# Optimization experiments

Measured on AMD Instinct MI355X. Metric: run time of the kernel, lower is better.

The kernel has to match this reference:

```python
import jax, jax.numpy as jnp
import numpy as np

HEADS = 8
EPS = 1e-6

def conv1x1(x, W, b):
    # x: [B,C,H,W], W: [O,C], b: [O]
    return jnp.einsum('oc,bchw->bohw', W, x) + b[None, :, None, None]

def cross_attn(qf, kf, vf, Wq, bq, Wk, bk, Wv, bv, Wo, bo):
    B, C, H, W = qf.shape
    hd = C // HEADS
    Q = conv1x1(qf, Wq, bq).reshape(B, HEADS, hd, H * W)
    K = conv1x1(kf, Wk, bk).reshape(B, HEADS, hd, H * W)
    V = conv1x1(vf, Wv, bv).reshape(B, HEADS, hd, H * W)
    # contraction over spatial dim -> [B, heads, hd, hd] scores (faithful to source einsum)
    scores = jnp.einsum('bnhd,bnkd->bnhk', Q, K) * (hd ** -0.5)
    attn = jax.nn.softmax(scores, axis=-1)
    out = jnp.einsum('bnhk,bnkd->bnhd', attn, V).reshape(B, C, H, W)
    return conv1x1(out, Wo, bo)

def se_block(x, W1, b1, W2, b2):
    pooled = jnp.mean(x, axis=(2, 3), keepdims=True)  # [B,C,1,1]
    y = jax.nn.relu(conv1x1(pooled, W1, b1))
    return jax.nn.sigmoid(conv1x1(y, W2, b2))

def l2norm_c(x):
    n = jnp.sqrt(jnp.sum(x * x, axis=1, keepdims=True))
    return x / (n + EPS)

def setup_inputs() -> dict:
    key = jax.random.key(0)
    ks = jax.random.split(key, 24)
    B, C, H, W = 8, 512, 64, 64
    r = 16
    s = 0.02
    inp = {
        'rgb_features': jax.random.normal(ks[0], (B, C, H, W), jnp.float32),
        'depth_features': jax.random.normal(ks[1], (B, C, H, W), jnp.float32),
        'lidar_features': jax.random.normal(ks[2], (B, C, H, W), jnp.float32),
        # 6 cross-modal attention modules, stacked (all same channel sizes)
        # order: rgb->depth, rgb->lidar, depth->rgb, depth->lidar, lidar->rgb, lidar->depth
        'attn_Wq': jax.random.normal(ks[3], (6, C, C), jnp.float32) * s,
        'attn_bq': jnp.zeros((6, C), jnp.float32),
        'attn_Wk': jax.random.normal(ks[4], (6, C, C), jnp.float32) * s,
        'attn_bk': jnp.zeros((6, C), jnp.float32),
        'attn_Wv': jax.random.normal(ks[5], (6, C, C), jnp.float32) * s,
        'attn_bv': jnp.zeros((6, C), jnp.float32),
        'attn_Wo': jax.random.normal(ks[6], (6, C, C), jnp.float32) * s,
        'attn_bo': jnp.zeros((6, C), jnp.float32),
        # SE blocks for rgb/depth/lidar, stacked
        'se_W1': jax.random.normal(ks[7], (3, C // r, C), jnp.float32) * s,
        'se_b1': jnp.zeros((3, C // r), jnp.float32),
        'se_W2': jax.random.normal(ks[8], (3, C, C // r), jnp.float32) * s,
        'se_b2': jnp.zeros((3, C), jnp.float32),
        'gate_W': jax.random.normal(ks[9], (3, 3 * C + 3), jnp.float32) * s,
        'gate_b': jnp.zeros((3,), jnp.float32),
        'fusion_W': jax.random.normal(ks[10], (3 * C, 3 * C), jnp.float32) * s,
        'fusion_b': jnp.zeros((3 * C,), jnp.float32),
    }
    return inp

def reference(rgb_features, depth_features, lidar_features,
              attn_Wq, attn_bq, attn_Wk, attn_bk, attn_Wv, attn_bv, attn_Wo, attn_bo,
              se_W1, se_b1, se_W2, se_b2, gate_W, gate_b, fusion_W, fusion_b):
    def ca(i, qf, kf, vf):
        return cross_attn(qf, kf, vf,
                          attn_Wq[i], attn_bq[i], attn_Wk[i], attn_bk[i],
                          attn_Wv[i], attn_bv[i], attn_Wo[i], attn_bo[i])
    rgb_cross = rgb_features + ca(0, rgb_features, depth_features, depth_features) \
                             + ca(1, rgb_features, lidar_features, lidar_features)
    depth_cross = depth_features + ca(2, depth_features, rgb_features, rgb_features) \
                                 + ca(3, depth_features, lidar_features, lidar_features)
    lidar_cross = lidar_features + ca(4, lidar_features, rgb_features, rgb_features) \
                                 + ca(5, lidar_features, depth_features, depth_features)

    rgb_refined = l2norm_c(rgb_cross * se_block(rgb_cross, se_W1[0], se_b1[0], se_W2[0], se_b2[0]))
    depth_refined = l2norm_c(depth_cross * se_block(depth_cross, se_W1[1], se_b1[1], se_W2[1], se_b2[1]))
    lidar_refined = l2norm_c(lidar_cross * se_block(lidar_cross, se_W1[2], se_b1[2], se_W2[2], se_b2[2]))

    B, C, H, W = rgb_features.shape
    depth_sparsity = jnp.mean((depth_features == 0).astype(jnp.float32), axis=(1, 2, 3), keepdims=True)
    rgb_variance = jnp.var(rgb_features, axis=(1, 2, 3), keepdims=True, ddof=1)
    lidar_sparsity = jnp.mean((lidar_features == 0).astype(jnp.float32), axis=(1, 2, 3), keepdims=True)
    quality = jnp.concatenate([depth_sparsity, rgb_variance, lidar_sparsity], axis=1)  # [B,3,1,1]
    quality = jnp.broadcast_to(quality, (B, 3, H, W))

    combined = jnp.concatenate([rgb_refined, depth_refined, lidar_refined], axis=1)
    combined_with_metrics = jnp.concatenate([combined, quality], axis=1)
    alpha = jax.nn.sigmoid(conv1x1(combined_with_metrics, gate_W, gate_b))  # [B,3,H,W]

    weighted = jnp.concatenate([
        rgb_refined * alpha[:, 0:1],
        depth_refined * alpha[:, 1:2],
        lidar_refined * alpha[:, 2:3],
    ], axis=1)
    return conv1x1(weighted, fusion_W, fusion_b)
```

## Files before the change

### kernel.cpp

```cpp
#include <hip/hip_runtime.h>
#include <hip/hip_bf16.h>
#include <stdint.h>

using bf16 = __hip_bfloat16;
typedef short bfrag8 __attribute__((ext_vector_type(8)));
typedef float f32x4 __attribute__((ext_vector_type(4)));

constexpr long OFF_XT   = 0L;
constexpr long OFF_XC   = 100663296L;
constexpr long OFF_WQ   = 201326592L;
constexpr long OFF_WK   = 204472320L;
constexpr long OFF_WVT  = 207618048L;
constexpr long OFF_WOB  = 210763776L;
constexpr long OFF_FW   = 213909504L;
constexpr long OFF_BO2  = 218628096L;
constexpr long OFF_POOL = 218646528L;
constexpr long OFF_SE   = 218695680L;
constexpr long OFF_QACC = 218744832L;
constexpr long OFF_CS   = 218745856L;
constexpr long OFF_GB   = 218795008L;
constexpr long OFF_ATT  = 231377920L;
constexpr long OFF_VST  = 234523648L;
constexpr long OFF_QST  = 435850240L;
constexpr long OFF_MVEC = 436243456L;

__device__ __forceinline__ void mfma_bf16(f32x4& c, bfrag8 a, bfrag8 b) {
  asm("v_mfma_f32_16x16x32_bf16 %0, %1, %2, %0" : "+v"(c) : "v"(a), "v"(b));
}

__device__ __forceinline__ void gload16(const void* g, void* l) {
  __builtin_amdgcn_global_load_lds(
      (__attribute__((address_space(1))) void*)(g),
      (__attribute__((address_space(3))) void*)(l), 16, 0, 0);
}

__device__ __forceinline__ float bf2f(short s) {
  union { uint32_t u; float f; } cv;
  cv.u = ((uint32_t)(unsigned short)s) << 16;
  return cv.f;
}

__device__ __forceinline__ void swz_mn(int gy, long& m0, long& n0) {
  const int gx = gridDim.x;
  const int orig = blockIdx.y * gx + blockIdx.x;
  const int q = (gx * gy) >> 3;
  const int wgid = (orig & 7) * q + (orig >> 3);
  m0 = (long)(wgid / gy) * 128;
  n0 = (long)(wgid % gy) * 128;
}

#define SWZ_OFF(r, kb) ((kb) ^ (((r) & 7) << 4))

__device__ __forceinline__ void bar256() {
  __builtin_amdgcn_sched_barrier(0);
  __builtin_amdgcn_s_barrier();
  __builtin_amdgcn_sched_barrier(0);
}

__device__ __forceinline__ void stage_half(const bf16* __restrict__ g, long ldg,
                                           char* slot, int t) {
#pragma unroll
  for (int j = 0; j < 2; ++j) {
    const int L = t * 16 + j * 8192;
    const int r = L >> 7;
    const int kb = (L & 127) ^ ((r & 7) << 4);
    gload16(g + (long)r * ldg + (kb >> 1), slot + L);
  }
}

template<int NT>
__device__ __forceinline__ void gemm256_core(
    const bf16* __restrict__ A, long lda,
    const bf16* __restrict__ B, long ldb,
    long m0, long n0, char* sm, f32x4 (&acc)[4][4][2])
{
  const int t = threadIdx.x;
  const int lane = t & 63, wid = t >> 6;
  const int wm = wid >> 2, wn = wid & 3;
  const int l16 = lane & 15, lk = lane >> 4;

  auto STAGE = [&](int mat, int hf, int kt) {
    const bool wrap = (kt >= NT);
    const int ktw = wrap ? kt - NT : kt;
    const int kp = ktw & 1;
    char* slot = wrap ? (sm + 131072)
                      : (mat == 0 ? sm + (kp * 2 + hf) * 16384
                                  : sm + 65536 + (kp * 2 + hf) * 16384);
    if (mat == 0)
      stage_half(A + (m0 + (long)hf * 128) * lda + ktw * 64, lda, slot, t);
    else
      stage_half(B + (n0 + (long)hf * 128) * ldb + ktw * 64, ldb, slot, t);
  };

  STAGE(0, 0, 0); STAGE(0, 1, 0); STAGE(1, 0, 0); STAGE(1, 1, 0);
  STAGE(1, 1, 1); STAGE(0, 1, 1);
  __builtin_amdgcn_sched_barrier(0);
  asm volatile("s_waitcnt vmcnt(4)" ::: "memory");
  bar256();

  constexpr int s_mat[8] = {0, 1, 1, 0, 0, 1, 1, 0};
  constexpr int s_hf[8]  = {0, 0, 1, 1, 0, 0, 1, 1};
  constexpr int s_dkt[8] = {1, 1, 2, 2, 2, 2, 3, 3};

  bfrag8 af[4][2], bfr0[2][2], bfr1[2][2];

  for (int i = 0; i < NT / 2; ++i) {
#pragma unroll
    for (int p = 0; p < 8; ++p) {
      const int q = p & 3, kp = p >> 2;
      const int ah = (q >= 2) ? 1 : 0;
      const int bh = (q == 1 || q == 2) ? 1 : 0;
      const char* Ab = sm + (kp * 2 + ah) * 16384;
      const char* Bb = sm + 65536 + (kp * 2 + bh) * 16384;
      if (q == 0 || q == 2) {
#pragma unroll
        for (int mf = 0; mf < 4; ++mf) {
          const int rowA = wm * 64 + mf * 16 + l16;
#pragma unroll
          for (int ks = 0; ks < 2; ++ks)
            af[mf][ks] = *(const bfrag8*)(Ab + rowA * 128 +
                                          SWZ_OFF(rowA, ks * 64 + lk * 16));
        }
      }
      if (q == 0) {
#pragma unroll
        for (int nf = 0; nf < 2; ++nf) {
          const int rowB = wn * 32 + nf * 16 + l16;
#pragma unroll
          for (int ks = 0; ks < 2; ++ks)
            bfr0[nf][ks] = *(const bfrag8*)(Bb + rowB * 128 +
                                            SWZ_OFF(rowB, ks * 64 + lk * 16));
        }
      }
      if (q == 1) {
#pragma unroll
        for (int nf = 0; nf < 2; ++nf) {
          const int rowB = wn * 32 + nf * 16 + l16;
#pragma unroll
          for (int ks = 0; ks < 2; ++ks)
            bfr1[nf][ks] = *(const bfrag8*)(Bb + rowB * 128 +
                                            SWZ_OFF(rowB, ks * 64 + lk * 16));
        }
      }
      STAGE(s_mat[p], s_hf[p], 2 * i + s_dkt[p]);
      bar256();
      __builtin_amdgcn_s_setprio(1);
      if (q == 0 || q == 3) {
#pragma unroll
        for (int ks = 0; ks < 2; ++ks)
#pragma unroll
          for (int mf = 0; mf < 4; ++mf)
#pragma unroll
            for (int nf = 0; nf < 2; ++nf)
              mfma_bf16(acc[q][mf][nf], af[mf][ks], bfr0[nf][ks]);
      } else {
#pragma unroll
        for (int ks = 0; ks < 2; ++ks)
#pragma unroll
          for (int mf = 0; mf < 4; ++mf)
#pragma unroll
            for (int nf = 0; nf < 2; ++nf)
              mfma_bf16(acc[q][mf][nf], af[mf][ks], bfr1[nf][ks]);
      }
      __builtin_amdgcn_s_setprio(0);
      if (p == 3 || p == 7) {
        __builtin_amdgcn_sched_barrier(0);
        asm volatile("s_waitcnt vmcnt(4)" ::: "memory");
      }
      bar256();
    }
  }
}

__global__ __launch_bounds__(512, 2) void fusion_gemm256(
    const bf16* __restrict__ A, const bf16* __restrict__ Bt,
    float* __restrict__ Cf, const float* __restrict__ bias)
{
  __shared__ __align__(16) char sm[147456];
  const int orig = blockIdx.y * 128 + blockIdx.x;
  const int wgid = (orig & 7) * 96 + (orig >> 3);
  const long m0 = (long)(wgid / 6) * 256;
  const long n0 = (long)(wgid % 6) * 256;
  f32x4 acc[4][4][2];
#pragma unroll
  for (int q = 0; q < 4; ++q)
#pragma unroll
    for (int mf = 0; mf < 4; ++mf)
#pragma unroll
      for (int nf = 0; nf < 2; ++nf)
        acc[q][mf][nf] = f32x4{0.f, 0.f, 0.f, 0.f};
  gemm256_core<24>(A, 1536, Bt, 1536, m0, n0, sm, acc);

  const int t = threadIdx.x;
  const int lane = t & 63, wid = t >> 6;
  const int wm = wid >> 2, wn = wid & 3;
  const int l16 = lane & 15, lk = lane >> 4;
  constexpr int s_ah[4] = {0, 0, 1, 1};
  constexpr int s_bh[4] = {0, 1, 1, 0};
  const long b = m0 >> 12;
#pragma unroll
  for (int q = 0; q < 4; ++q) {
    const int ah = s_ah[q], bh = s_bh[q];
#pragma unroll
    for (int mf = 0; mf < 4; ++mf) {
      const long row = m0 + ah * 128 + wm * 64 + mf * 16 + lk * 4;
      const long p = row & 4095;
#pragma unroll
      for (int nf = 0; nf < 2; ++nf) {
        const long gc = n0 + bh * 128 + wn * 32 + nf * 16 + l16;
        const float bb = bias[gc];
        float4 o4;
        o4.x = acc[q][mf][nf][0] + bb; o4.y = acc[q][mf][nf][1] + bb;
        o4.z = acc[q][mf][nf][2] + bb; o4.w = acc[q][mf][nf][3] + bb;
        *(float4*)(Cf + b * 6291456L + gc * 4096L + p) = o4;
      }
    }
  }
}

__global__ __launch_bounds__(256) void transpose_kernel(
    const float* __restrict__ x0, const float* __restrict__ x1,
    const float* __restrict__ x2, bf16* __restrict__ xT, bf16* __restrict__ xC,
    float* __restrict__ cs, float* __restrict__ qstage)
{
  __shared__ float tile[32][33];
  __shared__ float qpart[4][2];
  const int zz = blockIdx.z;
  const int m = zz >> 3, b = zz & 7;
  const float* x = (m == 0) ? x0 : (m == 1) ? x1 : x2;
  bf16* y = xT + (long)m * 16777216;
  bf16* y2 = xC + (long)m * 16777216;
  const int p0 = blockIdx.x * 32, c0 = blockIdx.y * 32;
  const int tx = threadIdx.x, ty = threadIdx.y;
  float csp[4];
  float qa = 0.f, qb_ = 0.f;
#pragma unroll
  for (int j = 0; j < 4; ++j) {
    const float v = x[((long)b * 512 + c0 + ty + j * 8) * 4096 + p0 + tx];
    tile[ty + j * 8][tx] = v;
    y2[(long)(c0 + ty + j * 8) * 32768 + (long)b * 4096 + p0 + tx] = __float2bfloat16(v);
    csp[j] = v;
    if (m == 0) { qa += v; qb_ += v * v; }
    else qa += (v == 0.0f) ? 1.0f : 0.0f;
  }
  __syncthreads();
#pragma unroll
  for (int j = 0; j < 4; ++j)
    y[((long)b * 4096 + p0 + ty + j * 8) * 512 + c0 + tx] =
        __float2bfloat16(tile[tx][ty + j * 8]);
#pragma unroll
  for (int j = 0; j < 4; ++j) {
    float s = csp[j];
    for (int o = 16; o; o >>= 1) s += __shfl_xor(s, o);
    if (tx == 0) atomicAdd(&cs[(m * 8 + b) * 512 + c0 + ty + j * 8], s);
  }
  const int t = ty * 32 + tx;
  const int lane = t & 63;
  for (int o = 32; o; o >>= 1) { qa += __shfl_xor(qa, o); qb_ += __shfl_xor(qb_, o); }
  if (lane == 0) { qpart[t >> 6][0] = qa; qpart[t >> 6][1] = qb_; }
  __syncthreads();
  if (t == 0) {
    const float pa = qpart[0][0] + qpart[1][0] + qpart[2][0] + qpart[3][0];
    const float pb = qpart[0][1] + qpart[1][1] + qpart[2][1] + qpart[3][1];
    float* qs = qstage + ((long)zz * 2048 + blockIdx.y * 128 + blockIdx.x) * 2;
    qs[0] = pa; qs[1] = pb;
  }
}

__global__ __launch_bounds__(256) void quality_reduce(
    const float* __restrict__ qstage, float* __restrict__ qacc)
{
  __shared__ float pr[4][2];
  const int zz = blockIdx.x;
  const int m = zz >> 3, b = zz & 7;
  const int t = threadIdx.x;
  float sa = 0.f, sb = 0.f;
  for (int i = t; i < 2048; i += 256) {
    sa += qstage[((long)zz * 2048 + i) * 2];
    sb += qstage[((long)zz * 2048 + i) * 2 + 1];
  }
  for (int o = 32; o; o >>= 1) { sa += __shfl_xor(sa, o); sb += __shfl_xor(sb, o); }
  if ((t & 63) == 0) { pr[t >> 6][0] = sa; pr[t >> 6][1] = sb; }
  __syncthreads();
  if (t == 0) {
    sa = pr[0][0] + pr[1][0] + pr[2][0] + pr[3][0];
    sb = pr[0][1] + pr[1][1] + pr[2][1] + pr[3][1];
    if (m == 0) { qacc[b * 4 + 1] = sa; qacc[b * 4 + 2] = sb; }
    else if (m == 1) qacc[b * 4 + 0] = sa;
    else qacc[b * 4 + 3] = sa;
  }
}

__global__ void prep_weights(
    const float* __restrict__ wq, const float* __restrict__ wk,
    const float* __restrict__ wv, const float* __restrict__ wo,
    const float* __restrict__ fw, const float* __restrict__ bo,
    bf16* __restrict__ wqB, bf16* __restrict__ wkB, bf16* __restrict__ wvT,
    bf16* __restrict__ woB, bf16* __restrict__ fwB, float* __restrict__ bo2)
{
  const long stride = (long)gridDim.x * blockDim.x;
  for (long j = (long)blockIdx.x * blockDim.x + threadIdx.x; j < 2359296; j += stride) {
    fwB[j] = __float2bfloat16(fw[j]);
    if (j < 1572864) {
      wqB[j] = __float2bfloat16(wq[j]);
      wkB[j] = __float2bfloat16(wk[j]);
      woB[j] = __float2bfloat16(wo[j]);
      const long i = j >> 18, rem = j & 262143, cin = rem >> 9, ef = rem & 511;
      wvT[j] = __float2bfloat16(wv[(i << 18) + (ef << 9) + cin]);
    }
    if (j < 1536) {
      const long m2 = j >> 9, cc = j & 511;
      bo2[j] = bo[((m2 * 2) << 9) + cc] + bo[((m2 * 2 + 1) << 9) + cc];
    }
  }
}

template<int BM, int BN>
__device__ __forceinline__ void gemm_core(
    const bf16* __restrict__ A, long lda,
    const bf16* __restrict__ Bt, long ldb,
    int K, long m0, long n0,
    bf16* As, bf16* Bs, f32x4 (&acc)[BM / 32][BN / 32])
{
  constexpr int WM = BM / 2, WN = BN / 2, FM = BM / 32, FN = BN / 32;
  const int t = threadIdx.x;
  const int lane = t & 63, wv = t >> 6;
  const int wr = wv >> 1, wc = wv & 1;
  const int l16 = lane & 15, lk = lane >> 4;
  const int srow = t >> 2;
  const int scol = (t & 3) * 8;
  const bf16* Ag = A + (m0 + srow) * lda + scol;
  const bf16* Bg = Bt + (n0 + srow) * ldb + scol;
  char* AsB = (char*)As;
  char* BsB = (char*)Bs;
  const int aoff = wv * 1024;
  for (int kk = 0; kk < K; kk += 32) {
#pragma unroll
    for (int it = 0; it < BM / 64; ++it)
      gload16(Ag + (long)it * 64 * lda + kk, AsB + it * 4096 + aoff);
#pragma unroll
    for (int it = 0; it < BN / 64; ++it)
      gload16(Bg + (long)it * 64 * ldb + kk, BsB + it * 4096 + aoff);
    __syncthreads();
    bfrag8 af[FM], bfr[FN];
#pragma unroll
    for (int m = 0; m < FM; ++m)
      af[m] = *(const bfrag8*)(AsB + ((wr * WM + m * 16 + l16) * 32 + lk * 8) * 2);
#pragma unroll
    for (int n = 0; n < FN; ++n)
      bfr[n] = *(const bfrag8*)(BsB + ((wc * WN + n * 16 + l16) * 32 + lk * 8) * 2);
#pragma unroll
    for (int m = 0; m < FM; ++m)
#pragma unroll
      for (int n = 0; n < FN; ++n)
        mfma_bf16(acc[m][n], af[m], bfr[n]);
    __syncthreads();
  }
}

__global__ __launch_bounds__(256, 2) void cross_gemm(
    const bf16* __restrict__ xT, const bf16* __restrict__ Weff,
    bf16* __restrict__ crossB, const float* __restrict__ bo2,
    const float* __restrict__ mvec, float* __restrict__ pooled)
{
  __shared__ __align__(16) bf16 As[128 * 32];
  __shared__ __align__(16) bf16 Bs[128 * 32];
  const int z = blockIdx.z;
  const int qm = z >> 3, b = z & 7;
  const int KM0[3] = {1, 0, 0}, KM1[3] = {2, 2, 1};
  const bf16* A0 = xT + (long)KM0[qm] * 16777216 + (long)b * 2097152;
  const bf16* A1 = xT + (long)KM1[qm] * 16777216 + (long)b * 2097152;
  const bf16* B0 = Weff + ((long)(2 * qm) * 8 + b) * 262144;
  const bf16* B1 = Weff + ((long)(2 * qm + 1) * 8 + b) * 262144;
  const bf16* residT = xT + (long)qm * 16777216;
  bf16* Cb = crossB + (long)qm * 16777216;
  f32x4 acc[4][4];
#pragma unroll
  for (int m = 0; m < 4; ++m)
#pragma unroll
    for (int n = 0; n < 4; ++n)
      acc[m][n] = f32x4{0.f, 0.f, 0.f, 0.f};
  long m0, n0;
  swz_mn(4, m0, n0);
  gemm_core<128, 128>(A0, 512, B0, 512, 512, m0, n0, As, Bs, acc);
  gemm_core<128, 128>(A1, 512, B1, 512, 512, m0, n0, As, Bs, acc);

  const int t = threadIdx.x;
  const int lane = t & 63, wv = t >> 6;
  const int wr = wv >> 1, wc = wv & 1;
  const int l16 = lane & 15, lk = lane >> 4;
  const float* mv0 = mvec + ((long)(2 * qm) * 8 + b) * 512;
  const float* mv1 = mvec + ((long)(2 * qm + 1) * 8 + b) * 512;
  float csum[4] = {0.f, 0.f, 0.f, 0.f};
#pragma unroll
  for (int m = 0; m < 4; ++m) {
    const long p = m0 + wr * 64 + m * 16 + lk * 4;
    const long gr0 = (long)b * 4096 + p;
#pragma unroll
    for (int n = 0; n < 4; ++n) {
      const long gc = n0 + wc * 64 + n * 16 + l16;
      const float bb = bo2[qm * 512 + gc] + mv0[gc] + mv1[gc];
#pragma unroll
      for (int i2 = 0; i2 < 4; ++i2) {
        const float rv = __bfloat162float(residT[(gr0 + i2) * 512 + gc]);
        const float o = acc[m][n][i2] + bb + rv;
        Cb[(gr0 + i2) * 512 + gc] = __float2bfloat16(o);
        csum[n] += o;
      }
    }
  }
#pragma unroll
  for (int n = 0; n < 4; ++n) {
    float s = csum[n];
    s += __shfl_xor(s, 16);
    s += __shfl_xor(s, 32);
    if (lane < 16) {
      const long gc = n0 + wc * 64 + n * 16 + l16;
      atomicAdd(&pooled[((long)qm * 8 + b) * 512 + gc], s);
    }
  }
}

__global__ __launch_bounds__(256, 2) void gram_kernel(
    const bf16* __restrict__ xC, bf16* __restrict__ Gb)
{
  __shared__ __align__(16) bf16 As[128 * 32];
  __shared__ __align__(16) bf16 Bs[128 * 32];
  const int z = blockIdx.z;
  const int pair = z >> 3, b = z & 7;
  const int A1[3] = {0, 0, 1}, A2[3] = {1, 2, 2};
  const bf16* A = xC + (long)A1[pair] * 16777216 + b * 4096;
  const bf16* Bt = xC + (long)A2[pair] * 16777216 + b * 4096;
  f32x4 acc[4][4];
#pragma unroll
  for (int m = 0; m < 4; ++m)
#pragma unroll
    for (int n = 0; n < 4; ++n)
      acc[m][n] = f32x4{0.f, 0.f, 0.f, 0.f};
  const long m0 = (long)blockIdx.x * 128, n0 = (long)blockIdx.y * 128;
  gemm_core<128, 128>(A, 32768, Bt, 32768, 4096, m0, n0, As, Bs, acc);
  bf16* C = Gb + (long)z * 262144;
  const int t = threadIdx.x;
  const int lane = t & 63, wv = t >> 6;
  const int wr = wv >> 1, wc = wv & 1;
  const int l16 = lane & 15, lk = lane >> 4;
#pragma unroll
  for (int m = 0; m < 4; ++m) {
    const long gr0 = m0 + wr * 64 + m * 16 + lk * 4;
#pragma unroll
    for (int n = 0; n < 4; ++n) {
      const long gc = n0 + wc * 64 + n * 16 + l16;
#pragma unroll
      for (int i = 0; i < 4; ++i)
        C[(gr0 + i) * 512 + gc] = __float2bfloat16(acc[m][n][i]);
    }
  }
}

__global__ __launch_bounds__(256, 2) void scores_kernel(
    const bf16* __restrict__ wqB, const bf16* __restrict__ wkB,
    const bf16* __restrict__ Gb, const float* __restrict__ colsum,
    const float* __restrict__ bq, const float* __restrict__ bk,
    bf16* __restrict__ attnT)
{
  __shared__ __align__(16) bf16 RtS[64 * 520];
  __shared__ float uv[128];
  __shared__ __align__(16) bf16 attT[64][64];
  const int h = blockIdx.x, b = blockIdx.y, i = blockIdx.z;
  const int qm = i >> 1, jj = i & 1;
  const int km = jj ? (qm == 2 ? 1 : 2) : (qm == 0 ? 1 : 0);
  const int lo = qm < km ? qm : km, hi = qm < km ? km : qm;
  const int pair = lo + hi - 1;
  const int trans = qm > km;
  const bf16* G = Gb + ((long)(pair * 8 + b)) * 262144;
  const bf16* Wq_h = wqB + (long)i * 262144 + h * 64 * 512;
  const bf16* Wk_h = wkB + (long)i * 262144 + h * 64 * 512;
  const bf16* WA = trans ? Wk_h : Wq_h;
  const bf16* WB = trans ? Wq_h : Wk_h;
  const int t = threadIdx.x, lane = t & 63, wv = t >> 6;
  const int l16 = lane & 15, lk = lane >> 4;

  if (t < 128) {
    const int d = t & 63;
    const bf16* wrow = ((t < 64) ? Wq_h : Wk_h) + d * 512;
    const float* sv = colsum + (((t < 64) ? qm : km) * 8 + b) * 512;
    float a = 0.f;
    for (int c = 0; c < 512; c += 8) {
      const bfrag8 w8 = *(const bfrag8*)(wrow + c);
#pragma unroll
      for (int e = 0; e < 8; ++e) a += bf2f(w8[e]) * sv[c + e];
    }
    uv[t] = a;
  }

  f32x4 acc[8][4];
#pragma unroll
  for (int m = 0; m < 8; ++m)
#pragma unroll
    for (int n = 0; n < 4; ++n)
      acc[m][n] = f32x4{0.f, 0.f, 0.f, 0.f};
  for (int kk = 0; kk < 512; kk += 32) {
    bfrag8 a[8], bb[4];
#pragma unroll
    for (int m = 0; m < 8; ++m)
      a[m] = *(const bfrag8*)(G + (wv * 128 + m * 16 + l16) * 512 + kk + lk * 8);
#pragma unroll
    for (int n = 0; n < 4; ++n)
      bb[n] = *(const bfrag8*)(WB + (n * 16 + l16) * 512 + kk + lk * 8);
#pragma unroll
    for (int m = 0; m < 8; ++m)
#pragma unroll
      for (int n = 0; n < 4; ++n)
        mfma_bf16(acc[m][n], a[m], bb[n]);
  }
#pragma unroll
  for (int m = 0; m < 8; ++m)
#pragma unroll
    for (int n = 0; n < 4; ++n)
#pragma unroll
      for (int idx = 0; idx < 4; ++idx)
        RtS[(n * 16 + l16) * 520 + wv * 128 + m * 16 + lk * 4 + idx] =
            __float2bfloat16(acc[m][n][idx]);
  __syncthreads();

  f32x4 acc2[4];
#pragma unroll
  for (int m = 0; m < 4; ++m) acc2[m] = f32x4{0.f, 0.f, 0.f, 0.f};
  for (int kk = 0; kk < 512; kk += 32) {
    bfrag8 a2[4];
#pragma unroll
    for (int m = 0; m < 4; ++m)
      a2[m] = *(const bfrag8*)(WA + (m * 16 + l16) * 512 + kk + lk * 8);
    const bfrag8 b2 = *(const bfrag8*)(&RtS[(wv * 16 + l16) * 520 + kk + lk * 8]);
#pragma unroll
    for (int m = 0; m < 4; ++m) mfma_bf16(acc2[m], a2[m], b2);
  }
  __syncthreads();
  float* S = (float*)RtS;
#pragma unroll
  for (int m = 0; m < 4; ++m)
#pragma unroll
    for (int idx = 0; idx < 4; ++idx)
      S[(m * 16 + lk * 4 + idx) * 68 + wv * 16 + l16] = acc2[m][idx];
  __syncthreads();

  const int r = t >> 2, q = t & 3;
  const float* bq_h = bq + i * 512 + h * 64;
  const float* bk_h = bk + i * 512 + h * 64;
  const float u_r = uv[r], bq_r = bq_h[r];
  float vals[16];
  float mx = -1e30f;
#pragma unroll
  for (int kq = 0; kq < 16; ++kq) {
    const int k = q * 16 + kq;
    float s = trans ? S[k * 68 + r] : S[r * 68 + k];
    s += u_r * bk_h[k] + bq_r * uv[64 + k] + 4096.0f * bq_r * bk_h[k];
    s *= 0.125f;
    vals[kq] = s;
    mx = fmaxf(mx, s);
  }
  mx = fmaxf(mx, __shfl_xor(mx, 1));
  mx = fmaxf(mx, __shfl_xor(mx, 2));
  float sum = 0.f;
#pragma unroll
  for (int kq = 0; kq < 16; ++kq) { vals[kq] = expf(vals[kq] - mx); sum += vals[kq]; }
  sum += __shfl_xor(sum, 1);
  sum += __shfl_xor(sum, 2);
  const float inv = 1.0f / sum;
#pragma unroll
  for (int kq = 0; kq < 16; ++kq)
    attT[q * 16 + kq][r] = __float2bfloat16(vals[kq] * inv);
  __syncthreads();
  const int er = t >> 2, c16 = (t & 3) * 16;
  bf16* op = attnT + (((long)(i * 8 + b) * 8 + h) * 64 + er) * 64 + c16;
  *(bfrag8*)(op) = *(const bfrag8*)(&attT[er][c16]);
  *(bfrag8*)(op + 8) = *(const bfrag8*)(&attT[er][c16 + 8]);
}

__global__ __launch_bounds__(256, 2) void mfold_kernel(
    const bf16* __restrict__ woB, const bf16* __restrict__ attnT,
    const float* __restrict__ bv, bf16* __restrict__ Mbuf, float* __restrict__ mvec)
{
  __shared__ __align__(16) bf16 As[128 * 32];
  __shared__ __align__(16) bf16 Bs[64 * 32];
  const int ib = blockIdx.z;
  const int i = ib >> 3;
  const int h = blockIdx.y;
  const bf16* A = woB + (long)i * 262144 + h * 64;
  const bf16* Bt = attnT + ((long)ib * 8 + h) * 4096;
  f32x4 acc[4][2];
#pragma unroll
  for (int m = 0; m < 4; ++m)
#pragma unroll
    for (int n = 0; n < 2; ++n)
      acc[m][n] = f32x4{0.f, 0.f, 0.f, 0.f};
  const long m0 = (long)blockIdx.x * 128;
  gemm_core<128, 64>(A, 512, Bt, 64, 64, m0, 0, As, Bs, acc);

  const int t = threadIdx.x;
  const int lane = t & 63, wv = t >> 6;
  const int wr = wv >> 1, wc = wv & 1;
  const int l16 = lane & 15, lk = lane >> 4;
  bf16* C = Mbuf + (long)ib * 262144;
  const float* bvp = bv + i * 512 + h * 64;
  float mp[4][4];
#pragma unroll
  for (int m = 0; m < 4; ++m)
#pragma unroll
    for (int i2 = 0; i2 < 4; ++i2) mp[m][i2] = 0.f;
#pragma unroll
  for (int m = 0; m < 4; ++m) {
    const long gr0 = m0 + wr * 64 + m * 16 + lk * 4;
#pragma unroll
    for (int n = 0; n < 2; ++n) {
      const int gc = wc * 32 + n * 16 + l16;
      const float bvv = bvp[gc];
#pragma unroll
      for (int i2 = 0; i2 < 4; ++i2) {
        C[(gr0 + i2) * 512 + h * 64 + gc] = __float2bfloat16(acc[m][n][i2]);
        mp[m][i2] += acc[m][n][i2] * bvv;
      }
    }
  }
#pragma unroll
  for (int m = 0; m < 4; ++m)
#pragma unroll
    for (int i2 = 0; i2 < 4; ++i2) {
      float v = mp[m][i2];
      v += __shfl_xor(v, 1); v += __shfl_xor(v, 2);
      v += __shfl_xor(v, 4); v += __shfl_xor(v, 8);
      if (l16 == 0)
        atomicAdd(&mvec[(long)ib * 512 + m0 + wr * 64 + m * 16 + lk * 4 + i2], v);
    }
}

__global__ __launch_bounds__(256, 2) void weff_gemm(
    const bf16* __restrict__ Mbuf, const bf16* __restrict__ wvT,
    bf16* __restrict__ Weff)
{
  __shared__ __align__(16) bf16 As[128 * 32];
  __shared__ __align__(16) bf16 Bs[128 * 32];
  const int ib = blockIdx.z;
  const int i = ib >> 3;
  f32x4 acc[4][4];
#pragma unroll
  for (int m = 0; m < 4; ++m)
#pragma unroll
    for (int n = 0; n < 4; ++n)
      acc[m][n] = f32x4{0.f, 0.f, 0.f, 0.f};
  const long m0 = (long)blockIdx.x * 128, n0 = (long)blockIdx.y * 128;
  gemm_core<128, 128>(Mbuf + (long)ib * 262144, 512, wvT + (long)i * 262144, 512,
                      512, m0, n0, As, Bs, acc);
  bf16* C = Weff + (long)ib * 262144;
  const int t = threadIdx.x;
  const int lane = t & 63, wv = t >> 6;
  const int wr = wv >> 1, wc = wv & 1;
  const int l16 = lane & 15, lk = lane >> 4;
#pragma unroll
  for (int m = 0; m < 4; ++m) {
    const long gr0 = m0 + wr * 64 + m * 16 + lk * 4;
#pragma unroll
    for (int n = 0; n < 4; ++n) {
      const long gc = n0 + wc * 64 + n * 16 + l16;
#pragma unroll
      for (int i2 = 0; i2 < 4; ++i2)
        C[(gr0 + i2) * 512 + gc] = __float2bfloat16(acc[m][n][i2]);
    }
  }
}

__global__ __launch_bounds__(512) void se_mlp(
    const float* __restrict__ pooled,
    const float* __restrict__ W1, const float* __restrict__ b1,
    const float* __restrict__ W2, const float* __restrict__ b2,
    float* __restrict__ se)
{
  const int b = blockIdx.x, m = blockIdx.y;
  __shared__ float y[32];
  const int t = threadIdx.x;
  if (t < 32) {
    float s = b1[m * 32 + t];
    const float* w = W1 + (long)(m * 32 + t) * 512;
    const float* p = pooled + ((long)m * 8 + b) * 512;
    for (int c = 0; c < 512; ++c) s += w[c] * (p[c] * (1.0f / 4096.0f));
    y[t] = fmaxf(s, 0.0f);
  }
  __syncthreads();
  float s = b2[m * 512 + t];
  const float* w2 = W2 + (long)(m * 512 + t) * 32;
#pragma unroll
  for (int j = 0; j < 32; ++j) s += w2[j] * y[j];
  se[((long)m * 8 + b) * 512 + t] = 1.0f / (1.0f + expf(-s));
}

__global__ __launch_bounds__(384) void refine_gate(
    const bf16* __restrict__ cr0, const bf16* __restrict__ cr1,
    const bf16* __restrict__ cr2, const float* __restrict__ se,
    const float* __restrict__ gw, const float* __restrict__ gb,
    const float* __restrict__ qacc, bf16* __restrict__ weighted)
{
  __shared__ float part[2][3][3];
  const int t = threadIdx.x, wv = t >> 6, lane = t & 63;
  const int px_i = (wv >= 3) ? 1 : 0;
  const int m = wv - px_i * 3;
  const int pix = blockIdx.x * 2 + px_i;
  const int b = pix >> 12;
  const bf16* cr = (m == 0) ? cr0 : (m == 1) ? cr1 : cr2;
  const int c0 = lane * 8;
  const bfrag8 v8 = *(const bfrag8*)(cr + (long)pix * 512 + c0);
  const float* sp = se + ((long)m * 8 + b) * 512 + c0;
  const float4 s0 = *(const float4*)(sp);
  const float4 s1 = *(const float4*)(sp + 4);
  float w[8] = {bf2f(v8[0]) * s0.x, bf2f(v8[1]) * s0.y,
                bf2f(v8[2]) * s0.z, bf2f(v8[3]) * s0.w,
                bf2f(v8[4]) * s1.x, bf2f(v8[5]) * s1.y,
                bf2f(v8[6]) * s1.z, bf2f(v8[7]) * s1.w};
  float ss = 0.f;
#pragma unroll
  for (int i = 0; i < 8; ++i) ss += w[i] * w[i];
  for (int o = 32; o; o >>= 1) ss += __shfl_xor(ss, o);
  const float inv = 1.0f / (sqrtf(ss) + 1e-6f);
  float rf[8];
#pragma unroll
  for (int i = 0; i < 8; ++i) rf[i] = w[i] * inv;

  float a0 = 0.f, a1 = 0.f, a2 = 0.f;
#pragma unroll
  for (int i = 0; i < 8; ++i) {
    const int c = m * 512 + c0 + i;
    a0 += gw[c] * rf[i];
    a1 += gw[1539 + c] * rf[i];
    a2 += gw[3078 + c] * rf[i];
  }
  for (int o = 32; o; o >>= 1) {
    a0 += __shfl_xor(a0, o); a1 += __shfl_xor(a1, o); a2 += __shfl_xor(a2, o);
  }
  if (lane == 0) {
    part[px_i][m][0] = a0; part[px_i][m][1] = a1; part[px_i][m][2] = a2;
  }
  __syncthreads();
  const float N = 2097152.0f;
  const float q0 = qacc[b * 4 + 0] / N;
  const float q1 = (qacc[b * 4 + 2] - qacc[b * 4 + 1] * qacc[b * 4 + 1] / N) / (N - 1.0f);
  const float q2 = qacc[b * 4 + 3] / N;
  const float sg = part[px_i][0][m] + part[px_i][1][m] + part[px_i][2][m] + gb[m] +
                   gw[m * 1539 + 1536] * q0 + gw[m * 1539 + 1537] * q1 +
                   gw[m * 1539 + 1538] * q2;
  const float al = 1.0f / (1.0f + expf(-sg));
  __align__(16) bf16 tmp[8];
#pragma unroll
  for (int i = 0; i < 8; ++i) tmp[i] = __float2bfloat16(rf[i] * al);
  *(bfrag8*)(weighted + (long)pix * 1536 + m * 512 + c0) = *(const bfrag8*)tmp;
}

extern "C" void kernel_launch(void* const* d_in, const int* in_sizes, int n_in,
                              void* d_out, int out_size, void* d_ws, size_t ws_size,
                              hipStream_t stream)
{
  (void)in_sizes; (void)n_in; (void)out_size; (void)ws_size;
  const float* rgb   = (const float*)d_in[0];
  const float* depth = (const float*)d_in[1];
  const float* lidar = (const float*)d_in[2];
  const float* wq  = (const float*)d_in[3];
  const float* bq  = (const float*)d_in[4];
  const float* wk  = (const float*)d_in[5];
  const float* bk  = (const float*)d_in[6];
  const float* wvw = (const float*)d_in[7];
  const float* bv  = (const float*)d_in[8];
  const float* wo  = (const float*)d_in[9];
  const float* bo  = (const float*)d_in[10];
  const float* seW1 = (const float*)d_in[11];
  const float* seb1 = (const float*)d_in[12];
  const float* seW2 = (const float*)d_in[13];
  const float* seb2 = (const float*)d_in[14];
  const float* gw  = (const float*)d_in[15];
  const float* gb  = (const float*)d_in[16];
  const float* fw  = (const float*)d_in[17];
  const float* fb  = (const float*)d_in[18];

  char* ws = (char*)d_ws;
  bf16*  xT   = (bf16*)(ws + OFF_XT);
  bf16*  xC   = (bf16*)(ws + OFF_XC);
  bf16*  wqB  = (bf16*)(ws + OFF_WQ);
  bf16*  wkB  = (bf16*)(ws + OFF_WK);
  bf16*  wvT  = (bf16*)(ws + OFF_WVT);
  bf16*  woB  = (bf16*)(ws + OFF_WOB);
  bf16*  fwB  = (bf16*)(ws + OFF_FW);
  float* bo2  = (float*)(ws + OFF_BO2);
  float* pooled = (float*)(ws + OFF_POOL);
  float* seB  = (float*)(ws + OFF_SE);
  float* qacc = (float*)(ws + OFF_QACC);
  float* cs   = (float*)(ws + OFF_CS);
  bf16*  Gb   = (bf16*)(ws + OFF_GB);
  bf16*  attnT = (bf16*)(ws + OFF_ATT);
  float* qstage = (float*)(ws + OFF_QST);
  float* mvec = (float*)(ws + OFF_MVEC);
  bf16*  Mbuf = (bf16*)(ws + OFF_XC);
  bf16*  Weff = (bf16*)(ws + OFF_XC + 25165824L);
  bf16*  crossB = (bf16*)(ws + OFF_VST);

  (void)hipMemsetAsync(ws + OFF_POOL, 0, OFF_CS + 49152 - OFF_POOL, stream);
  (void)hipMemsetAsync(ws + OFF_MVEC, 0, 98304, stream);

  transpose_kernel<<<dim3(128, 16, 24), dim3(32, 8), 0, stream>>>(rgb, depth, lidar,
                                                                  xT, xC, cs, qstage);
  quality_reduce<<<24, 256, 0, stream>>>(qstage, qacc);
  prep_weights<<<2048, 256, 0, stream>>>(wq, wk, wvw, wo, fw, bo,
                                         wqB, wkB, wvT, woB, fwB, bo2);

  gram_kernel<<<dim3(4, 4, 24), 256, 0, stream>>>(xC, Gb);
  scores_kernel<<<dim3(8, 8, 6), 256, 0, stream>>>(wqB, wkB, Gb, cs, bq, bk, attnT);

  mfold_kernel<<<dim3(4, 8, 48), 256, 0, stream>>>(woB, attnT, bv, Mbuf, mvec);
  weff_gemm<<<dim3(4, 4, 48), 256, 0, stream>>>(Mbuf, wvT, Weff);

  cross_gemm<<<dim3(32, 4, 24), 256, 0, stream>>>(xT, Weff, crossB, bo2, mvec, pooled);
  se_mlp<<<dim3(8, 3), 512, 0, stream>>>(pooled, seW1, seb1, seW2, seb2, seB);

  bf16* cross0 = crossB;
  bf16* cross1 = (bf16*)(ws + OFF_VST + 33554432L);
  bf16* cross2 = (bf16*)(ws + OFF_VST + 67108864L);
  bf16* weighted = (bf16*)(ws + OFF_XC);
  refine_gate<<<16384, 384, 0, stream>>>(cross0, cross1, cross2, seB, gw, gb, qacc, weighted);

  fusion_gemm256<<<dim3(128, 6), 512, 0, stream>>>(weighted, fwB, (float*)d_out, fb);
}
```

Baseline: 882.9 us.

## Move cross GEMM onto pipelined 256x256 core with identity-segment residual

Replaces the 128x128 cross_gemm with a 256x256-tile, 512-thread kernel built on the pipelined gemm256_core, which now takes several K segments from different base pointers. The residual add is folded into the GEMM as a third K segment, multiplying the query modality's features by a bf16 identity matrix built in prep_weights. This removes the separate residual read in the epilogue and gains the larger tile and deeper pipeline. The cost is 50% more MFMA work on an identity block, and the grid shrinks to 768 blocks, which may hurt occupancy balance.

```diff
diff --git a/kernel.cpp b/kernel.cpp
--- a/kernel.cpp
+++ b/kernel.cpp
@@ -23,6 +23,7 @@
 constexpr long OFF_VST  = 234523648L;
 constexpr long OFF_QST  = 435850240L;
 constexpr long OFF_MVEC = 436243456L;
+constexpr long OFF_IDB  = 436341760L;
 
 __device__ __forceinline__ void mfma_bf16(f32x4& c, bfrag8 a, bfrag8 b) {
   asm("v_mfma_f32_16x16x32_bf16 %0, %1, %2, %0" : "+v"(c) : "v"(a), "v"(b));
@@ -68,12 +69,13 @@
   }
 }
 
-template<int NT>
+template<int NSEG, int NTSEG>
 __device__ __forceinline__ void gemm256_core(
-    const bf16* __restrict__ A, long lda,
-    const bf16* __restrict__ B, long ldb,
+    const bf16* const* Aseg, long lda,
+    const bf16* const* Bseg, long ldb,
     long m0, long n0, char* sm, f32x4 (&acc)[4][4][2])
 {
+  constexpr int NT = NSEG * NTSEG;
   const int t = threadIdx.x;
   const int lane = t & 63, wid = t >> 6;
   const int wm = wid >> 2, wn = wid & 3;
@@ -82,14 +84,15 @@
   auto STAGE = [&](int mat, int hf, int kt) {
     const bool wrap = (kt >= NT);
     const int ktw = wrap ? kt - NT : kt;
+    const int seg = ktw / NTSEG, ktt = ktw % NTSEG;
     const int kp = ktw & 1;
     char* slot = wrap ? (sm + 131072)
                       : (mat == 0 ? sm + (kp * 2 + hf) * 16384
                                   : sm + 65536 + (kp * 2 + hf) * 16384);
     if (mat == 0)
-      stage_half(A + (m0 + (long)hf * 128) * lda + ktw * 64, lda, slot, t);
+      stage_half(Aseg[seg] + (m0 + (long)hf * 128) * lda + ktt * 64, lda, slot, t);
     else
-      stage_half(B + (n0 + (long)hf * 128) * ldb + ktw * 64, ldb, slot, t);
+      stage_half(Bseg[seg] + (n0 + (long)hf * 128) * ldb + ktt * 64, ldb, slot, t);
   };
 
   STAGE(0, 0, 0); STAGE(0, 1, 0); STAGE(1, 0, 0); STAGE(1, 1, 0);
@@ -189,7 +192,9 @@
 #pragma unroll
       for (int nf = 0; nf < 2; ++nf)
         acc[q][mf][nf] = f32x4{0.f, 0.f, 0.f, 0.f};
-  gemm256_core<24>(A, 1536, Bt, 1536, m0, n0, sm, acc);
+  const bf16* Aseg[1] = {A};
+  const bf16* Bseg[1] = {Bt};
+  gemm256_core<1, 24>(Aseg, 1536, Bseg, 1536, m0, n0, sm, acc);
 
   const int t = threadIdx.x;
   const int lane = t & 63, wid = t >> 6;
@@ -216,6 +221,82 @@
       }
     }
   }
+}
+
+__global__ __launch_bounds__(512, 2) void cross_gemm256(
+    const bf16* __restrict__ xT, const bf16* __restrict__ Weff,
+    const bf16* __restrict__ idB,
+    bf16* __restrict__ crossB, const float* __restrict__ bo2,
+    const float* __restrict__ mvec, float* __restrict__ pooled)
+{
+  __shared__ __align__(16) char sm[147456];
+  const int z = blockIdx.z;
+  const int qm = z >> 3, b = z & 7;
+  const int KM0[3] = {1, 0, 0}, KM1[3] = {2, 2, 1};
+  const bf16* Aseg[3] = {
+      xT + (long)KM0[qm] * 16777216 + (long)b * 2097152,
+      xT + (long)KM1[qm] * 16777216 + (long)b * 2097152,
+      xT + (long)qm * 16777216 + (long)b * 2097152};
+  const bf16* Bseg[3] = {
+      Weff + ((long)(2 * qm) * 8 + b) * 262144,
+      Weff + ((long)(2 * qm + 1) * 8 + b) * 262144,
+      idB};
+  const int orig = blockIdx.y * 16 + blockIdx.x;
+  const int wgid = (orig & 7) * 4 + (orig >> 3);
+  const long m0 = (long)(wgid >> 1) * 256;
+  const long n0 = (long)(wgid & 1) * 256;
+  f32x4 acc[4][4][2];
+#pragma unroll
+  for (int q = 0; q < 4; ++q)
+#pragma unroll
+    for (int mf = 0; mf < 4; ++mf)
+#pragma unroll
+      for (int nf = 0; nf < 2; ++nf)
+        acc[q][mf][nf] = f32x4{0.f, 0.f, 0.f, 0.f};
+  gemm256_core<3, 8>(Aseg, 512, Bseg, 512, m0, n0, sm, acc);
+
+  const int t = threadIdx.x;
+  const int lane = t & 63, wid = t >> 6;
+  const int wm = wid >> 2, wn = wid & 3;
+  const int l16 = lane & 15, lk = lane >> 4;
+  constexpr int s_ah[4] = {0, 0, 1, 1};
+  constexpr int s_bh[4] = {0, 1, 1, 0};
+  bf16* Cb = crossB + (long)qm * 16777216;
+  const float* mv0 = mvec + ((long)(2 * qm) * 8 + b) * 512;
+  const float* mv1 = mvec + ((long)(2 * qm + 1) * 8 + b) * 512;
+  float csum[2][2] = {{0.f, 0.f}, {0.f, 0.f}};
+#pragma unroll
+  for (int q = 0; q < 4; ++q) {
+    const int ah = s_ah[q], bh = s_bh[q];
+#pragma unroll
+    for (int mf = 0; mf < 4; ++mf) {
+      const long row = m0 + ah * 128 + wm * 64 + mf * 16 + lk * 4;
+      const long gr0 = (long)b * 4096 + row;
+#pragma unroll
+      for (int nf = 0; nf < 2; ++nf) {
+        const long gc = n0 + bh * 128 + wn * 32 + nf * 16 + l16;
+        const float bb = bo2[qm * 512 + gc] + mv0[gc] + mv1[gc];
+#pragma unroll
+        for (int i2 = 0; i2 < 4; ++i2) {
+          const float o = acc[q][mf][nf][i2] + bb;
+          Cb[(gr0 + i2) * 512 + gc] = __float2bfloat16(o);
+          csum[bh][nf] += o;
+        }
+      }
+    }
+  }
+#pragma unroll
+  for (int bh = 0; bh < 2; ++bh)
+#pragma unroll
+    for (int nf = 0; nf < 2; ++nf) {
+      float s = csum[bh][nf];
+      s += __shfl_xor(s, 16);
+      s += __shfl_xor(s, 32);
+      if (lk == 0) {
+        const long gc = n0 + bh * 128 + wn * 32 + nf * 16 + l16;
+        atomicAdd(&pooled[((long)qm * 8 + b) * 512 + gc], s);
+      }
+    }
 }
 
 __global__ __launch_bounds__(256) void transpose_kernel(
@@ -296,7 +377,8 @@
     const float* __restrict__ wv, const float* __restrict__ wo,
     const float* __restrict__ fw, const float* __restrict__ bo,
     bf16* __restrict__ wqB, bf16* __restrict__ wkB, bf16* __restrict__ wvT,
-    bf16* __restrict__ woB, bf16* __restrict__ fwB, float* __restrict__ bo2)
+    bf16* __restrict__ woB, bf16* __restrict__ fwB, float* __restrict__ bo2,
+    bf16* __restrict__ idB)
 {
   const long stride = (long)gridDim.x * blockDim.x;
   for (long j = (long)blockIdx.x * blockDim.x + threadIdx.x; j < 2359296; j += stride) {
@@ -307,6 +389,10 @@
       woB[j] = __float2bfloat16(wo[j]);
       const long i = j >> 18, rem = j & 262143, cin = rem >> 9, ef = rem & 511;
       wvT[j] = __float2bfloat16(wv[(i << 18) + (ef << 9) + cin]);
+    }
+    if (j < 262144) {
+      const long r = j >> 9, c = j & 511;
+      idB[j] = __float2bfloat16((r == c) ? 1.0f : 0.0f);
     }
     if (j < 1536) {
       const long m2 = j >> 9, cc = j & 511;
@@ -355,69 +441,6 @@
       for (int n = 0; n < FN; ++n)
         mfma_bf16(acc[m][n], af[m], bfr[n]);
     __syncthreads();
-  }
-}
-
-__global__ __launch_bounds__(256, 2) void cross_gemm(
-    const bf16* __restrict__ xT, const bf16* __restrict__ Weff,
-    bf16* __restrict__ crossB, const float* __restrict__ bo2,
-    const float* __restrict__ mvec, float* __restrict__ pooled)
-{
-  __shared__ __align__(16) bf16 As[128 * 32];
-  __shared__ __align__(16) bf16 Bs[128 * 32];
-  const int z = blockIdx.z;
-  const int qm = z >> 3, b = z & 7;
-  const int KM0[3] = {1, 0, 0}, KM1[3] = {2, 2, 1};
-  const bf16* A0 = xT + (long)KM0[qm] * 16777216 + (long)b * 2097152;
-  const bf16* A1 = xT + (long)KM1[qm] * 16777216 + (long)b * 2097152;
-  const bf16* B0 = Weff + ((long)(2 * qm) * 8 + b) * 262144;
-  const bf16* B1 = Weff + ((long)(2 * qm + 1) * 8 + b) * 262144;
-  const bf16* residT = xT + (long)qm * 16777216;
-  bf16* Cb = crossB + (long)qm * 16777216;
-  f32x4 acc[4][4];
-#pragma unroll
-  for (int m = 0; m < 4; ++m)
-#pragma unroll
-    for (int n = 0; n < 4; ++n)
-      acc[m][n] = f32x4{0.f, 0.f, 0.f, 0.f};
-  long m0, n0;
-  swz_mn(4, m0, n0);
-  gemm_core<128, 128>(A0, 512, B0, 512, 512, m0, n0, As, Bs, acc);
-  gemm_core<128, 128>(A1, 512, B1, 512, 512, m0, n0, As, Bs, acc);
-
-  const int t = threadIdx.x;
-  const int lane = t & 63, wv = t >> 6;
-  const int wr = wv >> 1, wc = wv & 1;
-  const int l16 = lane & 15, lk = lane >> 4;
-  const float* mv0 = mvec + ((long)(2 * qm) * 8 + b) * 512;
-  const float* mv1 = mvec + ((long)(2 * qm + 1) * 8 + b) * 512;
-  float csum[4] = {0.f, 0.f, 0.f, 0.f};
-#pragma unroll
-  for (int m = 0; m < 4; ++m) {
-    const long p = m0 + wr * 64 + m * 16 + lk * 4;
-    const long gr0 = (long)b * 4096 + p;
-#pragma unroll
-    for (int n = 0; n < 4; ++n) {
-      const long gc = n0 + wc * 64 + n * 16 + l16;
-      const float bb = bo2[qm * 512 + gc] + mv0[gc] + mv1[gc];
-#pragma unroll
-      for (int i2 = 0; i2 < 4; ++i2) {
-        const float rv = __bfloat162float(residT[(gr0 + i2) * 512 + gc]);
-        const float o = acc[m][n][i2] + bb + rv;
-        Cb[(gr0 + i2) * 512 + gc] = __float2bfloat16(o);
-        csum[n] += o;
-      }
-    }
-  }
-#pragma unroll
-  for (int n = 0; n < 4; ++n) {
-    float s = csum[n];
-    s += __shfl_xor(s, 16);
-    s += __shfl_xor(s, 32);
-    if (lane < 16) {
-      const long gc = n0 + wc * 64 + n * 16 + l16;
-      atomicAdd(&pooled[((long)qm * 8 + b) * 512 + gc], s);
-    }
   }
 }
 
@@ -795,6 +818,7 @@
   bf16*  attnT = (bf16*)(ws + OFF_ATT);
   float* qstage = (float*)(ws + OFF_QST);
   float* mvec = (float*)(ws + OFF_MVEC);
+  bf16*  idB  = (bf16*)(ws + OFF_IDB);
   bf16*  Mbuf = (bf16*)(ws + OFF_XC);
   bf16*  Weff = (bf16*)(ws + OFF_XC + 25165824L);
   bf16*  crossB = (bf16*)(ws + OFF_VST);
@@ -806,7 +830,7 @@
                                                                   xT, xC, cs, qstage);
   quality_reduce<<<24, 256, 0, stream>>>(qstage, qacc);
   prep_weights<<<2048, 256, 0, stream>>>(wq, wk, wvw, wo, fw, bo,
-                                         wqB, wkB, wvT, woB, fwB, bo2);
+                                         wqB, wkB, wvT, woB, fwB, bo2, idB);
 
   gram_kernel<<<dim3(4, 4, 24), 256, 0, stream>>>(xC, Gb);
   scores_kernel<<<dim3(8, 8, 6), 256, 0, stream>>>(wqB, wkB, Gb, cs, bq, bk, attnT);
@@ -814,7 +838,8 @@
   mfold_kernel<<<dim3(4, 8, 48), 256, 0, stream>>>(woB, attnT, bv, Mbuf, mvec);
   weff_gemm<<<dim3(4, 4, 48), 256, 0, stream>>>(Mbuf, wvT, Weff);
 
-  cross_gemm<<<dim3(32, 4, 24), 256, 0, stream>>>(xT, Weff, crossB, bo2, mvec, pooled);
+  cross_gemm256<<<dim3(16, 2, 24), 512, 0, stream>>>(xT, Weff, idB, crossB, bo2,
+                                                     mvec, pooled);
   se_mlp<<<dim3(8, 3), 512, 0, stream>>>(pooled, seW1, seb1, seW2, seb2, seB);
 
   bf16* cross0 = crossB;
```

After: 807.4 us. -8.6%, faster.
